# Optimization experiments

Measured on AMD Instinct MI355X. Metric: run time of the kernel, lower is better.

Reference implementation:

```python
import jax, jax.numpy as jnp
import numpy as np

N = 50000
E = 800000
IN_FEAT = 128
HEADS = 2
HEAD_DIM = 64  # hidden_feat // num_heads for 'concat'
HIDDEN = HEADS * HEAD_DIM
N_CLASSES = 16
NEG_SLOPE = 0.2
BN_EPS = 1e-5


def setup_inputs() -> dict:
    key = jax.random.key(0)
    ks = jax.random.split(key, 20)
    s = 0.1  # weight scale for numerical sanity
    return {
        "x": jax.random.normal(ks[0], (N, IN_FEAT), jnp.float32),
        "src0": jax.random.randint(ks[1], (E,), 0, N, jnp.int32),
        "dst0": jax.random.randint(ks[2], (E,), 0, N, jnp.int32),
        "ew0": jax.random.uniform(ks[3], (E,), jnp.float32),
        "src1": jax.random.randint(ks[4], (E,), 0, N, jnp.int32),
        "dst1": jax.random.randint(ks[5], (E,), 0, N, jnp.int32),
        "ew1": jax.random.uniform(ks[6], (E,), jnp.float32),
        "fc_w0": jax.random.normal(ks[7], (HIDDEN, IN_FEAT), jnp.float32) * s,
        "bias0": jnp.zeros((HIDDEN,), jnp.float32),
        "attn_l0": jax.random.normal(ks[8], (HEADS, HEAD_DIM), jnp.float32) * s,
        "attn_r0": jax.random.normal(ks[9], (HEADS, HEAD_DIM), jnp.float32) * s,
        "fc_w1": jax.random.normal(ks[10], (HIDDEN, IN_FEAT), jnp.float32) * s,
        "bias1": jnp.zeros((HIDDEN,), jnp.float32),
        "attn_l1": jax.random.normal(ks[11], (HEADS, HEAD_DIM), jnp.float32) * s,
        "attn_r1": jax.random.normal(ks[12], (HEADS, HEAD_DIM), jnp.float32) * s,
        "skip_w": jax.random.normal(ks[13], (HIDDEN, IN_FEAT), jnp.float32) * s,
        "skip_b": jnp.zeros((HIDDEN,), jnp.float32),
        "bn_gamma": jnp.ones((HIDDEN,), jnp.float32),
        "bn_beta": jnp.zeros((HIDDEN,), jnp.float32),
        "clf_w": jax.random.normal(ks[14], (N_CLASSES, HIDDEN), jnp.float32) * s,
        "clf_b": jnp.zeros((N_CLASSES,), jnp.float32),
    }


def _weighted_gat(x, src, dst, ew, fc_w, bias, attn_l, attn_r):
    # DGL GATConv with per-edge weight scaling of attention.
    f = (x @ fc_w.T).reshape(N, HEADS, HEAD_DIM)          # [N,H,D]
    el = jnp.sum(f * attn_l, axis=-1)                      # [N,H]
    er = jnp.sum(f * attn_r, axis=-1)                      # [N,H]
    e = jax.nn.leaky_relu(el[src] + er[dst], NEG_SLOPE)    # [E,H]
    # edge softmax over incoming edges of each dst, numerically stable
    m = jax.ops.segment_max(e, dst, num_segments=N)        # [N,H]
    ex = jnp.exp(e - m[dst])
    den = jax.ops.segment_sum(ex, dst, num_segments=N)     # [N,H]
    alpha = ex / den[dst]                                  # [E,H]
    alpha = alpha * ew[:, None]                            # edge-weight scaling
    msg = alpha[..., None] * f[src]                        # [E,H,D]
    out = jax.ops.segment_sum(msg, dst, num_segments=N)    # [N,H,D]
    return out + bias.reshape(1, HEADS, HEAD_DIM)


def reference(x, src0, dst0, ew0, src1, dst1, ew1,
              fc_w0, bias0, attn_l0, attn_r0,
              fc_w1, bias1, attn_l1, attn_r1,
              skip_w, skip_b, bn_gamma, bn_beta, clf_w, clf_b):
    # HeteroGraphConv with aggregate='sum': sum per-relation GAT outputs
    h2 = _weighted_gat(x, src0, dst0, ew0, fc_w0, bias0, attn_l0, attn_r0) \
       + _weighted_gat(x, src1, dst1, ew1, fc_w1, bias1, attn_l1, attn_r1)
    # multihead 'concat' aggregate with relu: flatten heads
    h2 = jax.nn.relu(h2).reshape(N, HIDDEN)
    # linear skip + residual add (dropout is identity at eval)
    h = (x @ skip_w.T + skip_b) + h2
    # classifier: BatchNorm1d (batch stats) -> ReLU -> Linear
    mu = jnp.mean(h, axis=0)
    var = jnp.mean((h - mu) ** 2, axis=0)
    hn = (h - mu) * jax.lax.rsqrt(var + BN_EPS) * bn_gamma + bn_beta
    logits = jax.nn.relu(hn) @ clf_w.T + clf_b
    return logits
```

## Files before the change

### kernel.cpp

```cpp
#include <hip/hip_runtime.h>
#include <hip/hip_bf16.h>

#define N_NODES 50000
#define N_EDGES 800000
#define HID 128
#define NEG_SLOPE 0.2f
#define BN_EPS 1e-5f

#define NBLK 256
#define BINSZ 512
#define BINSH 9
#define NBINS 98

typedef __bf16 v8bf __attribute__((ext_vector_type(8)));
typedef float v4f __attribute__((ext_vector_type(4)));

__device__ __forceinline__ float leaky(float v) {
    return (v > 0.f) ? v : v * NEG_SLOPE;
}
__device__ __forceinline__ unsigned int f2bu(float f) {
    __hip_bfloat16 b = __float2bfloat16(f);
    return (unsigned int)*reinterpret_cast<unsigned short*>(&b);
}
__device__ __forceinline__ unsigned int pack2bf(float lo, float hi) {
    return f2bu(lo) | (f2bu(hi) << 16);
}

__global__ __launch_bounds__(256) void k_prepw(const float* __restrict__ w0,
                                               const float* __restrict__ w1,
                                               const float* __restrict__ wsk,
                                               unsigned short* __restrict__ wb) {
    const int WQ = 128 * 128 / 4;
    int q = blockIdx.x * 256 + threadIdx.x;
    if (q >= 3 * WQ) return;
    int mat = q >> 12;
    int rem = q & 4095;
    const float* W = (mat == 0) ? w0 : (mat == 1) ? w1 : wsk;
    float4 v = ((const float4*)W)[rem];
    ushort4 o;
    o.x = (unsigned short)f2bu(v.x);
    o.y = (unsigned short)f2bu(v.y);
    o.z = (unsigned short)f2bu(v.z);
    o.w = (unsigned short)f2bu(v.w);
    *(ushort4*)(wb + (size_t)mat * 16384 + rem * 4) = o;
}

__global__ __launch_bounds__(256) void k_bincount(const int* __restrict__ dst0,
                                                  const int* __restrict__ dst1,
                                                  int* __restrict__ bincnt) {
    int rel = blockIdx.y;
    const int* dst = rel ? dst1 : dst0;
    __shared__ int cnt[NBINS];
    for (int i = threadIdx.x; i < NBINS; i += 256) cnt[i] = 0;
    __syncthreads();
    const int CH = (N_EDGES + NBLK - 1) / NBLK;
    int b0 = blockIdx.x * CH;
    int b1 = min(N_EDGES, b0 + CH);
    for (int e = b0 + threadIdx.x; e < b1; e += 256)
        atomicAdd(&cnt[dst[e] >> BINSH], 1);
    __syncthreads();
    for (int i = threadIdx.x; i < NBINS; i += 256)
        bincnt[rel * NBINS * NBLK + i * NBLK + blockIdx.x] = cnt[i];
}

__global__ __launch_bounds__(1024) void k_binscan(int* __restrict__ bincnt) {
    int* a = bincnt + blockIdx.x * NBINS * NBLK;
    const int TOT = NBINS * NBLK;
    const int CH = (TOT + 1023) / 1024;
    int tid = threadIdx.x;
    int base = tid * CH;
    int lv[CH];
    int sum = 0;
    for (int i = 0; i < CH; i++) {
        int idx = base + i;
        int v = (idx < TOT) ? a[idx] : 0;
        lv[i] = sum;
        sum += v;
    }
    __shared__ int ls[1024];
    ls[tid] = sum;
    __syncthreads();
    for (int ofs = 1; ofs < 1024; ofs <<= 1) {
        int v = (tid >= ofs) ? ls[tid - ofs] : 0;
        __syncthreads();
        ls[tid] += v;
        __syncthreads();
    }
    int pre = tid ? ls[tid - 1] : 0;
    for (int i = 0; i < CH; i++) {
        int idx = base + i;
        if (idx < TOT) a[idx] = pre + lv[i];
    }
}

__global__ __launch_bounds__(256) void k_binscatter(const int* __restrict__ dst0,
                                                    const int* __restrict__ dst1,
                                                    const int* __restrict__ src0,
                                                    const int* __restrict__ src1,
                                                    const float* __restrict__ ew0,
                                                    const float* __restrict__ ew1,
                                                    const int* __restrict__ bincnt,
                                                    int2* __restrict__ pairs0,
                                                    int2* __restrict__ pairs1) {
    int rel = blockIdx.y;
    const int* dst = rel ? dst1 : dst0;
    const int* src = rel ? src1 : src0;
    const float* ew = rel ? ew1 : ew0;
    int2* pairs = rel ? pairs1 : pairs0;
    __shared__ int cur[NBINS];
    for (int i = threadIdx.x; i < NBINS; i += 256)
        cur[i] = bincnt[rel * NBINS * NBLK + i * NBLK + blockIdx.x];
    __syncthreads();
    const int CH = (N_EDGES + NBLK - 1) / NBLK;
    int b0 = blockIdx.x * CH;
    int b1 = min(N_EDGES, b0 + CH);
    for (int e = b0 + threadIdx.x; e < b1; e += 256) {
        int d = dst[e];
        int pos = atomicAdd(&cur[d >> BINSH], 1);
        unsigned int packed = (unsigned int)(d & (BINSZ - 1)) |
                              ((unsigned int)src[e] << BINSH);
        pairs[pos] = make_int2((int)packed, __float_as_int(ew[e]));
    }
}

__global__ __launch_bounds__(256) void k_csr(const int* __restrict__ bincnt,
                                             const int2* __restrict__ pairs0,
                                             const int2* __restrict__ pairs1,
                                             const float* __restrict__ el0,
                                             const float* __restrict__ el1,
                                             int* __restrict__ offs0,
                                             int* __restrict__ offs1,
                                             int4* __restrict__ rec0,
                                             int4* __restrict__ rec1) {
    int rel = blockIdx.y;
    const int2* pairs = rel ? pairs1 : pairs0;
    const float* el = rel ? el1 : el0;
    int* offs = rel ? offs1 : offs0;
    int4* rec = rel ? rec1 : rec0;
    int bin = blockIdx.x;
    int tid = threadIdx.x;
    const int* bc = bincnt + rel * NBINS * NBLK;
    int pbase = bc[bin * NBLK];
    int pend = (bin < NBINS - 1) ? bc[(bin + 1) * NBLK] : N_EDGES;
    int n0 = bin << BINSH;
    int nn = min(N_NODES - n0, BINSZ);

    __shared__ int s_deg[BINSZ];
    __shared__ int s_ts[256];
    for (int i = tid; i < BINSZ; i += 256) s_deg[i] = 0;
    __syncthreads();
    for (int p = pbase + tid; p < pend; p += 256)
        atomicAdd(&s_deg[((unsigned int)pairs[p].x) & (BINSZ - 1)], 1);
    __syncthreads();

    int d0 = s_deg[tid * 2], d1 = s_deg[tid * 2 + 1];
    s_ts[tid] = d0 + d1;
    __syncthreads();
    for (int ofs = 1; ofs < 256; ofs <<= 1) {
        int v = (tid >= ofs) ? s_ts[tid - ofs] : 0;
        __syncthreads();
        s_ts[tid] += v;
        __syncthreads();
    }
    int pre = tid ? s_ts[tid - 1] : 0;
    s_deg[tid * 2] = pbase + pre;
    s_deg[tid * 2 + 1] = pbase + pre + d0;
    __syncthreads();

    for (int l = tid; l < nn; l += 256) offs[n0 + l] = s_deg[l];
    if (bin == NBINS - 1 && tid == 0) offs[N_NODES] = N_EDGES;
    __syncthreads();

    for (int p = pbase + tid; p < pend; p += 256) {
        int2 pr = pairs[p];
        unsigned int u = (unsigned int)pr.x;
        int dl = (int)(u & (BINSZ - 1));
        int s = (int)(u >> BINSH);
        int pos = atomicAdd(&s_deg[dl], 1);
        float2 ev = *(const float2*)(el + 2 * s);
        rec[pos] = make_int4(s << 8, pr.y,
                             __float_as_int(ev.x), __float_as_int(ev.y));
    }
}

__global__ __launch_bounds__(256) void k_gemm_mfma(
    const float* __restrict__ x, const unsigned short* __restrict__ wb,
    const float* __restrict__ skip_b,
    const float* __restrict__ al0, const float* __restrict__ ar0,
    const float* __restrict__ al1, const float* __restrict__ ar1,
    unsigned short* __restrict__ fb0, unsigned short* __restrict__ fb1,
    float* __restrict__ el0, float* __restrict__ er0,
    float* __restrict__ el1, float* __restrict__ er1,
    float* __restrict__ hs) {
    __shared__ unsigned short As[64][128];
    __shared__ unsigned short Bs[64][128];
    int tid = threadIdx.x;
    int m0 = blockIdx.x * 64;

#pragma unroll
    for (int i = 0; i < 4; i++) {
        int idx = tid * 4 + i;
        int row = idx >> 4, seg = idx & 15;
        int gr = m0 + row;
        uint4 o = make_uint4(0, 0, 0, 0);
        if (gr < N_NODES) {
            const float* p = x + (size_t)gr * HID + seg * 8;
            float4 p0 = *(const float4*)p;
            float4 p1 = *(const float4*)(p + 4);
            o.x = pack2bf(p0.x, p0.y);
            o.y = pack2bf(p0.z, p0.w);
            o.z = pack2bf(p1.x, p1.y);
            o.w = pack2bf(p1.z, p1.w);
        }
        *(uint4*)(&As[row][(seg ^ (row & 7)) * 8]) = o;
    }
    __syncthreads();

    int w = tid >> 6, l = tid & 63;
    int lr = l & 15, lg = l >> 4;
    int node = m0 + w * 16 + lr;
    bool valid = node < N_NODES;
    int arow = w * 16 + lr;
    v8bf afrag[4];
#pragma unroll
    for (int kb = 0; kb < 4; kb++)
        afrag[kb] = *(v8bf*)(&As[arow][((kb * 4 + lg) ^ (arow & 7)) * 8]);

    for (int s = 0; s < 6; s++) {
        int mat = s >> 1;
        int j0 = (s & 1) * 64;
        const unsigned short* wmat = wb + (size_t)mat * 16384 + j0 * HID;
        __syncthreads();
#pragma unroll
        for (int i = 0; i < 4; i++) {
            int idx = tid * 4 + i;
            int row = idx >> 4, seg = idx & 15;
            uint4 wv = *(const uint4*)(wmat + row * HID + seg * 8);
            *(uint4*)(&Bs[row][(seg ^ (row & 7)) * 8]) = wv;
        }
        __syncthreads();

        v4f acc[4] = {};
#pragma unroll
        for (int nt = 0; nt < 4; nt++) {
            int brow = nt * 16 + lr;
#pragma unroll
            for (int kb = 0; kb < 4; kb++) {
                v8bf bfrag =
                    *(v8bf*)(&Bs[brow][((kb * 4 + lg) ^ (brow & 7)) * 8]);
                acc[nt] = __builtin_amdgcn_mfma_f32_16x16x32_bf16(
                    bfrag, afrag[kb], acc[nt], 0, 0, 0);
            }
        }

        if (mat < 2) {
            int h = s & 1;
            const float* al = mat ? al1 : al0;
            const float* ar = mat ? ar1 : ar0;
            float* elp = mat ? el1 : el0;
            float* erp = mat ? er1 : er0;
            unsigned short* fbp = mat ? fb1 : fb0;
            float elv = 0.f, erv = 0.f;
#pragma unroll
            for (int nt = 0; nt < 4; nt++) {
                int c0 = j0 + nt * 16 + lg * 4;
                float4 av = *(const float4*)(al + c0);
                float4 rv = *(const float4*)(ar + c0);
                elv += acc[nt][0] * av.x + acc[nt][1] * av.y +
                       acc[nt][2] * av.z + acc[nt][3] * av.w;
                erv += acc[nt][0] * rv.x + acc[nt][1] * rv.y +
                       acc[nt][2] * rv.z + acc[nt][3] * rv.w;
            }
            elv += __shfl_xor(elv, 16);
            elv += __shfl_xor(elv, 32);
            erv += __shfl_xor(erv, 16);
            erv += __shfl_xor(erv, 32);
            if (valid) {
#pragma unroll
                for (int nt = 0; nt < 4; nt++) {
                    uint2 o;
                    o.x = pack2bf(acc[nt][0], acc[nt][1]);
                    o.y = pack2bf(acc[nt][2], acc[nt][3]);
                    *(uint2*)(fbp + (size_t)node * HID + j0 + nt * 16 + lg * 4) = o;
                }
                if (lg == 0) {
                    elp[node * 2 + h] = elv;
                    erp[node * 2 + h] = erv;
                }
            }
        } else if (valid) {
#pragma unroll
            for (int nt = 0; nt < 4; nt++) {
                int c0 = j0 + nt * 16 + lg * 4;
                float4 sb = *(const float4*)(skip_b + c0);
                float4 o;
                o.x = acc[nt][0] + sb.x;
                o.y = acc[nt][1] + sb.y;
                o.z = acc[nt][2] + sb.z;
                o.w = acc[nt][3] + sb.w;
                *(float4*)(hs + (size_t)node * HID + c0) = o;
            }
        }
    }
}

__device__ __forceinline__ void agg_rel2(const int* __restrict__ offs,
                                         const int4* __restrict__ rec,
                                         const float* __restrict__ er,
                                         const unsigned char* __restrict__ fbb,
                                         int n, int lane, int sub8,
                                         int hh, float* a) {
    int b = offs[n];
    int e_end = offs[n + 1];
    int deg = e_end - b;
    if (deg <= 0) return;
    float ern0 = er[2 * n], ern1 = er[2 * n + 1];

    const int NC = 4;
    int cs[NC];
    float cw0[NC], cw1[NC];
    unsigned int cpk[NC];
    float d0 = 0.f, d1 = 0.f;
    int nchunk = (deg + 63) >> 6;
    for (int ch = 0; ch < nchunk; ch++) {
        int p = b + (ch << 6) + lane;
        int s = 0;
        float w0 = 0.f, w1 = 0.f;
        if (p < e_end) {
            int4 r = rec[p];
            s = r.x;
            float wgt = __int_as_float(r.y);
            float x0 = expf(leaky(__int_as_float(r.z) + ern0));
            float x1 = expf(leaky(__int_as_float(r.w) + ern1));
            d0 += x0;
            d1 += x1;
            w0 = x0 * wgt;
            w1 = x1 * wgt;
        }
        if (ch < NC) {
            cs[ch] = s;
            cw0[ch] = w0;
            cw1[ch] = w1;
        }
    }
#pragma unroll
    for (int m = 32; m; m >>= 1) {
        d0 += __shfl_xor(d0, m);
        d1 += __shfl_xor(d1, m);
    }
    float inv0 = 1.f / d0, inv1 = 1.f / d1;
#pragma unroll
    for (int ch = 0; ch < NC; ch++)
        cpk[ch] = pack2bf(cw0[ch] * inv0, cw1[ch] * inv1);

    for (int ch = 0; ch < nchunk; ch++) {
        int s;
        unsigned int pk;
        if (ch < NC) {
            s = cs[ch];
            pk = cpk[ch];
        } else {
            int p = b + (ch << 6) + lane;
            s = 0;
            pk = 0;
            if (p < e_end) {
                int4 r = rec[p];
                s = r.x;
                float wgt = __int_as_float(r.y);
                float w0 = expf(leaky(__int_as_float(r.z) + ern0)) * wgt;
                float w1 = expf(leaky(__int_as_float(r.w) + ern1)) * wgt;
                pk = pack2bf(w0 * inv0, w1 * inv1);
            }
        }
        int cnt = deg - (ch << 6);
        if (cnt > 64) cnt = 64;
        int ng = (cnt + 7) >> 3;
#pragma unroll 2
        for (int g = 0; g < ng; g++) {
            int sl = (g << 3) + sub8;
            int sj = __shfl(s, sl);
            unsigned int pkj = (unsigned int)__shfl((int)pk, sl);
            float aj = __uint_as_float(hh ? (pkj & 0xffff0000u) : (pkj << 16));
            uint4 f0 = *(const uint4*)(fbb + sj);
            uint4 f1 = *(const uint4*)(fbb + sj + 16);
            a[0]  += aj * __uint_as_float(f0.x << 16);
            a[1]  += aj * __uint_as_float(f0.x & 0xffff0000u);
            a[2]  += aj * __uint_as_float(f0.y << 16);
            a[3]  += aj * __uint_as_float(f0.y & 0xffff0000u);
            a[4]  += aj * __uint_as_float(f0.z << 16);
            a[5]  += aj * __uint_as_float(f0.z & 0xffff0000u);
            a[6]  += aj * __uint_as_float(f0.w << 16);
            a[7]  += aj * __uint_as_float(f0.w & 0xffff0000u);
            a[8]  += aj * __uint_as_float(f1.x << 16);
            a[9]  += aj * __uint_as_float(f1.x & 0xffff0000u);
            a[10] += aj * __uint_as_float(f1.y << 16);
            a[11] += aj * __uint_as_float(f1.y & 0xffff0000u);
            a[12] += aj * __uint_as_float(f1.z << 16);
            a[13] += aj * __uint_as_float(f1.z & 0xffff0000u);
            a[14] += aj * __uint_as_float(f1.w << 16);
            a[15] += aj * __uint_as_float(f1.w & 0xffff0000u);
        }
    }
}

__global__ __launch_bounds__(256) void k_aggregate(
    const int* __restrict__ offs0, const int4* __restrict__ rec0,
    const float* __restrict__ er0, const unsigned short* __restrict__ fb0,
    const int* __restrict__ offs1, const int4* __restrict__ rec1,
    const float* __restrict__ er1, const unsigned short* __restrict__ fb1,
    const float* __restrict__ bias0, const float* __restrict__ bias1,
    float* __restrict__ h) {
    int wave = threadIdx.x >> 6, lane = threadIdx.x & 63;
    int n = blockIdx.x * 4 + wave;
    if (n >= N_NODES) return;
    int cb8 = lane & 7;
    int sub8 = lane >> 3;
    int hh = cb8 >> 2;
    float a[16] = {};
    const unsigned char* fbb0 = (const unsigned char*)fb0 + cb8 * 32;
    const unsigned char* fbb1 = (const unsigned char*)fb1 + cb8 * 32;
    agg_rel2(offs0, rec0, er0, fbb0, n, lane, sub8, hh, a);
    agg_rel2(offs1, rec1, er1, fbb1, n, lane, sub8, hh, a);
#pragma unroll
    for (int j = 0; j < 16; j++) {
        a[j] += __shfl_xor(a[j], 8);
        a[j] += __shfl_xor(a[j], 16);
        a[j] += __shfl_xor(a[j], 32);
    }
    if (sub8 == 0) {
        int c0 = cb8 * 16;
        size_t base = (size_t)n * HID + c0;
#pragma unroll
        for (int q = 0; q < 4; q++) {
            float4 v = *(const float4*)(h + base + q * 4);
            float4 b0 = *(const float4*)(bias0 + c0 + q * 4);
            float4 b1 = *(const float4*)(bias1 + c0 + q * 4);
            float4 o;
            o.x = v.x + fmaxf(a[q * 4 + 0] + b0.x + b1.x, 0.f);
            o.y = v.y + fmaxf(a[q * 4 + 1] + b0.y + b1.y, 0.f);
            o.z = v.z + fmaxf(a[q * 4 + 2] + b0.z + b1.z, 0.f);
            o.w = v.w + fmaxf(a[q * 4 + 3] + b0.w + b1.w, 0.f);
            *(float4*)(h + base + q * 4) = o;
        }
    }
}

__global__ __launch_bounds__(256) void k_bnstats(const float* __restrict__ h,
                                                 double* __restrict__ psum,
                                                 double* __restrict__ psumsq) {
    int tid = threadIdx.x;
    const float4* h4 = (const float4*)h;
    double s[4] = {0.0, 0.0, 0.0, 0.0};
    double q[4] = {0.0, 0.0, 0.0, 0.0};
    const int totalv = N_NODES * HID / 4;
    const int stride = 512 * 256;
    for (int i = blockIdx.x * 256 + tid; i < totalv; i += stride) {
        float4 v = h4[i];
        s[0] += v.x; q[0] += (double)v.x * v.x;
        s[1] += v.y; q[1] += (double)v.y * v.y;
        s[2] += v.z; q[2] += (double)v.z * v.z;
        s[3] += v.w; q[3] += (double)v.w * v.w;
    }
    __shared__ double ls[256][4], lq[256][4];
#pragma unroll
    for (int j = 0; j < 4; j++) {
        ls[tid][j] = s[j];
        lq[tid][j] = q[j];
    }
    __syncthreads();
    if (tid < 32) {
#pragma unroll
        for (int j = 0; j < 4; j++) {
            double ss = 0.0, qq = 0.0;
            for (int t = tid; t < 256; t += 32) {
                ss += ls[t][j];
                qq += lq[t][j];
            }
            psum[blockIdx.x * 128 + tid * 4 + j] = ss;
            psumsq[blockIdx.x * 128 + tid * 4 + j] = qq;
        }
    }
}

__global__ void k_bn_finalize(const double* __restrict__ psum,
                              const double* __restrict__ psumsq,
                              const float* __restrict__ gamma,
                              const float* __restrict__ beta,
                              float* __restrict__ ss) {
    int c = threadIdx.x;
    double s = 0.0, q = 0.0;
    for (int b = 0; b < 512; b++) {
        s += psum[b * 128 + c];
        q += psumsq[b * 128 + c];
    }
    double mu = s / N_NODES;
    double var = q / N_NODES - mu * mu;
    float sc = gamma[c] * (float)(1.0 / sqrt(var + (double)BN_EPS));
    ss[c] = sc;
    ss[128 + c] = beta[c] - (float)mu * sc;
}

__global__ __launch_bounds__(256) void k_classify(const float* __restrict__ h,
                                                  const float* __restrict__ ss,
                                                  const float* __restrict__ clf_w,
                                                  const float* __restrict__ clf_b,
                                                  float* __restrict__ out) {
    int w = threadIdx.x >> 6, l = threadIdx.x & 63;
    int lr = l & 15, lg = l >> 4;
    int n0 = (blockIdx.x * 4 + w) * 16;
    if (n0 >= N_NODES) return;

    v8bf afrag[4], bfrag[4];
#pragma unroll
    for (int kb = 0; kb < 4; kb++) {
        int k0 = kb * 32 + lg * 8;
        const float* bp = clf_w + lr * HID + k0;
        float4 b0 = *(const float4*)bp;
        float4 b1 = *(const float4*)(bp + 4);
        bfrag[kb][0] = (__bf16)b0.x; bfrag[kb][1] = (__bf16)b0.y;
        bfrag[kb][2] = (__bf16)b0.z; bfrag[kb][3] = (__bf16)b0.w;
        bfrag[kb][4] = (__bf16)b1.x; bfrag[kb][5] = (__bf16)b1.y;
        bfrag[kb][6] = (__bf16)b1.z; bfrag[kb][7] = (__bf16)b1.w;
        const float* ap = h + (size_t)(n0 + lr) * HID + k0;
        float4 a0 = *(const float4*)ap;
        float4 a1 = *(const float4*)(ap + 4);
        float4 sc0 = *(const float4*)(ss + k0);
        float4 sc1 = *(const float4*)(ss + k0 + 4);
        float4 sh0 = *(const float4*)(ss + 128 + k0);
        float4 sh1 = *(const float4*)(ss + 128 + k0 + 4);
        afrag[kb][0] = (__bf16)fmaxf(a0.x * sc0.x + sh0.x, 0.f);
        afrag[kb][1] = (__bf16)fmaxf(a0.y * sc0.y + sh0.y, 0.f);
        afrag[kb][2] = (__bf16)fmaxf(a0.z * sc0.z + sh0.z, 0.f);
        afrag[kb][3] = (__bf16)fmaxf(a0.w * sc0.w + sh0.w, 0.f);
        afrag[kb][4] = (__bf16)fmaxf(a1.x * sc1.x + sh1.x, 0.f);
        afrag[kb][5] = (__bf16)fmaxf(a1.y * sc1.y + sh1.y, 0.f);
        afrag[kb][6] = (__bf16)fmaxf(a1.z * sc1.z + sh1.z, 0.f);
        afrag[kb][7] = (__bf16)fmaxf(a1.w * sc1.w + sh1.w, 0.f);
    }
    v4f acc = {};
#pragma unroll
    for (int kb = 0; kb < 4; kb++)
        acc = __builtin_amdgcn_mfma_f32_16x16x32_bf16(bfrag[kb], afrag[kb],
                                                      acc, 0, 0, 0);
    float4 cb = *(const float4*)(clf_b + lg * 4);
    float4 o;
    o.x = acc[0] + cb.x;
    o.y = acc[1] + cb.y;
    o.z = acc[2] + cb.z;
    o.w = acc[3] + cb.w;
    *(float4*)(out + (size_t)(n0 + lr) * 16 + lg * 4) = o;
}

extern "C" void kernel_launch(void* const* d_in, const int* in_sizes, int n_in,
                              void* d_out, int out_size, void* d_ws, size_t ws_size,
                              hipStream_t stream) {
    (void)in_sizes; (void)n_in; (void)out_size; (void)ws_size;
    const float* x      = (const float*)d_in[0];
    const int*   src0   = (const int*)d_in[1];
    const int*   dst0   = (const int*)d_in[2];
    const float* ew0    = (const float*)d_in[3];
    const int*   src1   = (const int*)d_in[4];
    const int*   dst1   = (const int*)d_in[5];
    const float* ew1    = (const float*)d_in[6];
    const float* fc_w0  = (const float*)d_in[7];
    const float* bias0  = (const float*)d_in[8];
    const float* al0    = (const float*)d_in[9];
    const float* ar0    = (const float*)d_in[10];
    const float* fc_w1  = (const float*)d_in[11];
    const float* bias1  = (const float*)d_in[12];
    const float* al1    = (const float*)d_in[13];
    const float* ar1    = (const float*)d_in[14];
    const float* skip_w = (const float*)d_in[15];
    const float* skip_b = (const float*)d_in[16];
    const float* gamma  = (const float*)d_in[17];
    const float* beta   = (const float*)d_in[18];
    const float* clf_w  = (const float*)d_in[19];
    const float* clf_b  = (const float*)d_in[20];
    float* out = (float*)d_out;

    char* wsp = (char*)d_ws;
    size_t off = 0;
    auto alloc = [&](size_t bytes) -> char* {
        char* p = wsp + off;
        off += (bytes + 255) & ~(size_t)255;
        return p;
    };
    unsigned short* wbf = (unsigned short*)alloc((size_t)3 * 16384 * 2);
    unsigned short* fb0 = (unsigned short*)alloc((size_t)N_NODES * HID * 2);
    unsigned short* fb1 = (unsigned short*)alloc((size_t)N_NODES * HID * 2);
    float*  hs     = (float*)alloc((size_t)N_NODES * HID * 4);
    float*  el0    = (float*)alloc((size_t)N_NODES * 2 * 4);
    float*  er0    = (float*)alloc((size_t)N_NODES * 2 * 4);
    float*  el1    = (float*)alloc((size_t)N_NODES * 2 * 4);
    float*  er1    = (float*)alloc((size_t)N_NODES * 2 * 4);
    int*    bincnt = (int*)alloc((size_t)2 * NBINS * NBLK * 4);
    int2*   pairs0 = (int2*)alloc((size_t)N_EDGES * 8);
    int2*   pairs1 = (int2*)alloc((size_t)N_EDGES * 8);
    int*    offs0  = (int*)alloc((size_t)(N_NODES + 1) * 4);
    int*    offs1  = (int*)alloc((size_t)(N_NODES + 1) * 4);
    int4*   rec0   = (int4*)alloc((size_t)N_EDGES * 16);
    int4*   rec1   = (int4*)alloc((size_t)N_EDGES * 16);
    double* psum   = (double*)alloc((size_t)512 * 128 * 8);
    double* psumsq = (double*)alloc((size_t)512 * 128 * 8);
    float*  ss     = (float*)alloc(256 * 4);

    k_prepw<<<48, 256, 0, stream>>>(fc_w0, fc_w1, skip_w, wbf);

    dim3 gbin(NBLK, 2);
    k_bincount<<<gbin, 256, 0, stream>>>(dst0, dst1, bincnt);
    k_binscan<<<2, 1024, 0, stream>>>(bincnt);
    k_binscatter<<<gbin, 256, 0, stream>>>(dst0, dst1, src0, src1, ew0, ew1,
                                           bincnt, pairs0, pairs1);

    k_gemm_mfma<<<(N_NODES + 63) / 64, 256, 0, stream>>>(
        x, wbf, skip_b, al0, ar0, al1, ar1,
        fb0, fb1, el0, er0, el1, er1, hs);

    dim3 gcsr(NBINS, 2);
    k_csr<<<gcsr, 256, 0, stream>>>(bincnt, pairs0, pairs1, el0, el1,
                                    offs0, offs1, rec0, rec1);

    k_aggregate<<<(N_NODES + 3) / 4, 256, 0, stream>>>(
        offs0, rec0, er0, fb0, offs1, rec1, er1, fb1, bias0, bias1, hs);

    k_bnstats<<<512, 256, 0, stream>>>(hs, psum, psumsq);
    k_bn_finalize<<<1, 128, 0, stream>>>(psum, psumsq, gamma, beta, ss);
    k_classify<<<(N_NODES + 63) / 64, 256, 0, stream>>>(
        hs, ss, clf_w, clf_b, out);
}
```

Before: 231.2 us.

## Precompute softmax numerators and denominators in CSR build, shrink edge records

Moves the edge exp(leaky(el+er)) computation and the per-destination softmax denominator accumulation into the CSR construction kernel, using shared-memory atomics. The edge record shrinks from 16 to 8 bytes by storing bf16-packed weighted numerators. The aggregation kernel becomes a single pass per chunk, with no second rec read or reduction. It also rebalances lanes to 16 columns by 4 edge groups with 16-byte gathers. The cost is that numerators are rounded to bf16 before normalization, and k_csr does extra shared atomics and er loads.

```diff
diff --git a/kernel.cpp b/kernel.cpp
--- a/kernel.cpp
+++ b/kernel.cpp
@@ -127,16 +127,22 @@
                                              const int2* __restrict__ pairs0,
                                              const int2* __restrict__ pairs1,
                                              const float* __restrict__ el0,
+                                             const float* __restrict__ er0,
                                              const float* __restrict__ el1,
+                                             const float* __restrict__ er1,
                                              int* __restrict__ offs0,
                                              int* __restrict__ offs1,
-                                             int4* __restrict__ rec0,
-                                             int4* __restrict__ rec1) {
+                                             int2* __restrict__ rec0,
+                                             int2* __restrict__ rec1,
+                                             float2* __restrict__ den20,
+                                             float2* __restrict__ den21) {
     int rel = blockIdx.y;
     const int2* pairs = rel ? pairs1 : pairs0;
     const float* el = rel ? el1 : el0;
+    const float* er = rel ? er1 : er0;
     int* offs = rel ? offs1 : offs0;
-    int4* rec = rel ? rec1 : rec0;
+    int2* rec = rel ? rec1 : rec0;
+    float2* den2 = rel ? den21 : den20;
     int bin = blockIdx.x;
     int tid = threadIdx.x;
     const int* bc = bincnt + rel * NBINS * NBLK;
@@ -147,7 +153,9 @@
 
     __shared__ int s_deg[BINSZ];
     __shared__ int s_ts[256];
+    __shared__ float sden[BINSZ * 2];
     for (int i = tid; i < BINSZ; i += 256) s_deg[i] = 0;
+    for (int i = tid; i < BINSZ * 2; i += 256) sden[i] = 0.f;
     __syncthreads();
     for (int p = pbase + tid; p < pend; p += 256)
         atomicAdd(&s_deg[((unsigned int)pairs[p].x) & (BINSZ - 1)], 1);
@@ -178,9 +186,17 @@
         int s = (int)(u >> BINSH);
         int pos = atomicAdd(&s_deg[dl], 1);
         float2 ev = *(const float2*)(el + 2 * s);
-        rec[pos] = make_int4(s << 8, pr.y,
-                             __float_as_int(ev.x), __float_as_int(ev.y));
-    }
+        float2 rv = *(const float2*)(er + 2 * (n0 + dl));
+        float x0 = expf(leaky(ev.x + rv.x));
+        float x1 = expf(leaky(ev.y + rv.y));
+        atomicAdd(&sden[dl * 2], x0);
+        atomicAdd(&sden[dl * 2 + 1], x1);
+        float ew = __int_as_float(pr.y);
+        rec[pos] = make_int2(s << 8, (int)pack2bf(x0 * ew, x1 * ew));
+    }
+    __syncthreads();
+    for (int l = tid; l < nn; l += 256)
+        den2[n0 + l] = make_float2(sden[l * 2], sden[l * 2 + 1]);
 }
 
 __global__ __launch_bounds__(256) void k_gemm_mfma(
@@ -305,143 +321,91 @@
 }
 
 __device__ __forceinline__ void agg_rel2(const int* __restrict__ offs,
-                                         const int4* __restrict__ rec,
-                                         const float* __restrict__ er,
+                                         const int2* __restrict__ rec,
+                                         const float2* __restrict__ den2,
                                          const unsigned char* __restrict__ fbb,
-                                         int n, int lane, int sub8,
+                                         int n, int lane, int sub,
                                          int hh, float* a) {
     int b = offs[n];
     int e_end = offs[n + 1];
     int deg = e_end - b;
     if (deg <= 0) return;
-    float ern0 = er[2 * n], ern1 = er[2 * n + 1];
-
-    const int NC = 4;
-    int cs[NC];
-    float cw0[NC], cw1[NC];
-    unsigned int cpk[NC];
-    float d0 = 0.f, d1 = 0.f;
+    float2 dn = den2[n];
+    float inv0 = 1.f / dn.x, inv1 = 1.f / dn.y;
+
     int nchunk = (deg + 63) >> 6;
     for (int ch = 0; ch < nchunk; ch++) {
         int p = b + (ch << 6) + lane;
         int s = 0;
-        float w0 = 0.f, w1 = 0.f;
+        unsigned int wpk = 0;
         if (p < e_end) {
-            int4 r = rec[p];
+            int2 r = rec[p];
             s = r.x;
-            float wgt = __int_as_float(r.y);
-            float x0 = expf(leaky(__int_as_float(r.z) + ern0));
-            float x1 = expf(leaky(__int_as_float(r.w) + ern1));
-            d0 += x0;
-            d1 += x1;
-            w0 = x0 * wgt;
-            w1 = x1 * wgt;
-        }
-        if (ch < NC) {
-            cs[ch] = s;
-            cw0[ch] = w0;
-            cw1[ch] = w1;
-        }
-    }
-#pragma unroll
-    for (int m = 32; m; m >>= 1) {
-        d0 += __shfl_xor(d0, m);
-        d1 += __shfl_xor(d1, m);
-    }
-    float inv0 = 1.f / d0, inv1 = 1.f / d1;
-#pragma unroll
-    for (int ch = 0; ch < NC; ch++)
-        cpk[ch] = pack2bf(cw0[ch] * inv0, cw1[ch] * inv1);
-
-    for (int ch = 0; ch < nchunk; ch++) {
-        int s;
-        unsigned int pk;
-        if (ch < NC) {
-            s = cs[ch];
-            pk = cpk[ch];
-        } else {
-            int p = b + (ch << 6) + lane;
-            s = 0;
-            pk = 0;
-            if (p < e_end) {
-                int4 r = rec[p];
-                s = r.x;
-                float wgt = __int_as_float(r.y);
-                float w0 = expf(leaky(__int_as_float(r.z) + ern0)) * wgt;
-                float w1 = expf(leaky(__int_as_float(r.w) + ern1)) * wgt;
-                pk = pack2bf(w0 * inv0, w1 * inv1);
-            }
-        }
+            wpk = (unsigned int)r.y;
+        }
+        unsigned int pk = pack2bf(__uint_as_float(wpk << 16) * inv0,
+                                  __uint_as_float(wpk & 0xffff0000u) * inv1);
         int cnt = deg - (ch << 6);
         if (cnt > 64) cnt = 64;
-        int ng = (cnt + 7) >> 3;
+        int ng = (cnt + 3) >> 2;
 #pragma unroll 2
         for (int g = 0; g < ng; g++) {
-            int sl = (g << 3) + sub8;
+            int sl = (g << 2) + sub;
             int sj = __shfl(s, sl);
             unsigned int pkj = (unsigned int)__shfl((int)pk, sl);
             float aj = __uint_as_float(hh ? (pkj & 0xffff0000u) : (pkj << 16));
-            uint4 f0 = *(const uint4*)(fbb + sj);
-            uint4 f1 = *(const uint4*)(fbb + sj + 16);
-            a[0]  += aj * __uint_as_float(f0.x << 16);
-            a[1]  += aj * __uint_as_float(f0.x & 0xffff0000u);
-            a[2]  += aj * __uint_as_float(f0.y << 16);
-            a[3]  += aj * __uint_as_float(f0.y & 0xffff0000u);
-            a[4]  += aj * __uint_as_float(f0.z << 16);
-            a[5]  += aj * __uint_as_float(f0.z & 0xffff0000u);
-            a[6]  += aj * __uint_as_float(f0.w << 16);
-            a[7]  += aj * __uint_as_float(f0.w & 0xffff0000u);
-            a[8]  += aj * __uint_as_float(f1.x << 16);
-            a[9]  += aj * __uint_as_float(f1.x & 0xffff0000u);
-            a[10] += aj * __uint_as_float(f1.y << 16);
-            a[11] += aj * __uint_as_float(f1.y & 0xffff0000u);
-            a[12] += aj * __uint_as_float(f1.z << 16);
-            a[13] += aj * __uint_as_float(f1.z & 0xffff0000u);
-            a[14] += aj * __uint_as_float(f1.w << 16);
-            a[15] += aj * __uint_as_float(f1.w & 0xffff0000u);
+            uint4 fv = *(const uint4*)(fbb + sj);
+            a[0] += aj * __uint_as_float(fv.x << 16);
+            a[1] += aj * __uint_as_float(fv.x & 0xffff0000u);
+            a[2] += aj * __uint_as_float(fv.y << 16);
+            a[3] += aj * __uint_as_float(fv.y & 0xffff0000u);
+            a[4] += aj * __uint_as_float(fv.z << 16);
+            a[5] += aj * __uint_as_float(fv.z & 0xffff0000u);
+            a[6] += aj * __uint_as_float(fv.w << 16);
+            a[7] += aj * __uint_as_float(fv.w & 0xffff0000u);
         }
     }
 }
 
 __global__ __launch_bounds__(256) void k_aggregate(
-    const int* __restrict__ offs0, const int4* __restrict__ rec0,
-    const float* __restrict__ er0, const unsigned short* __restrict__ fb0,
-    const int* __restrict__ offs1, const int4* __restrict__ rec1,
-    const float* __restrict__ er1, const unsigned short* __restrict__ fb1,
+    const int* __restrict__ offs0, const int2* __restrict__ rec0,
+    const float2* __restrict__ den20, const unsigned short* __restrict__ fb0,
+    const int* __restrict__ offs1, const int2* __restrict__ rec1,
+    const float2* __restrict__ den21, const unsigned short* __restrict__ fb1,
     const float* __restrict__ bias0, const float* __restrict__ bias1,
     float* __restrict__ h) {
     int wave = threadIdx.x >> 6, lane = threadIdx.x & 63;
     int n = blockIdx.x * 4 + wave;
     if (n >= N_NODES) return;
-    int cb8 = lane & 7;
-    int sub8 = lane >> 3;
-    int hh = cb8 >> 2;
-    float a[16] = {};
-    const unsigned char* fbb0 = (const unsigned char*)fb0 + cb8 * 32;
-    const unsigned char* fbb1 = (const unsigned char*)fb1 + cb8 * 32;
-    agg_rel2(offs0, rec0, er0, fbb0, n, lane, sub8, hh, a);
-    agg_rel2(offs1, rec1, er1, fbb1, n, lane, sub8, hh, a);
-#pragma unroll
-    for (int j = 0; j < 16; j++) {
-        a[j] += __shfl_xor(a[j], 8);
+    int cb = lane & 15;
+    int sub = lane >> 4;
+    int hh = cb >> 3;
+    float a[8] = {0.f, 0.f, 0.f, 0.f, 0.f, 0.f, 0.f, 0.f};
+    const unsigned char* fbb0 = (const unsigned char*)fb0 + cb * 16;
+    const unsigned char* fbb1 = (const unsigned char*)fb1 + cb * 16;
+    agg_rel2(offs0, rec0, den20, fbb0, n, lane, sub, hh, a);
+    agg_rel2(offs1, rec1, den21, fbb1, n, lane, sub, hh, a);
+#pragma unroll
+    for (int j = 0; j < 8; j++) {
         a[j] += __shfl_xor(a[j], 16);
         a[j] += __shfl_xor(a[j], 32);
     }
-    if (sub8 == 0) {
-        int c0 = cb8 * 16;
-        size_t base = (size_t)n * HID + c0;
-#pragma unroll
-        for (int q = 0; q < 4; q++) {
-            float4 v = *(const float4*)(h + base + q * 4);
-            float4 b0 = *(const float4*)(bias0 + c0 + q * 4);
-            float4 b1 = *(const float4*)(bias1 + c0 + q * 4);
-            float4 o;
-            o.x = v.x + fmaxf(a[q * 4 + 0] + b0.x + b1.x, 0.f);
-            o.y = v.y + fmaxf(a[q * 4 + 1] + b0.y + b1.y, 0.f);
-            o.z = v.z + fmaxf(a[q * 4 + 2] + b0.z + b1.z, 0.f);
-            o.w = v.w + fmaxf(a[q * 4 + 3] + b0.w + b1.w, 0.f);
-            *(float4*)(h + base + q * 4) = o;
-        }
+    if (sub == 0) {
+        size_t base = (size_t)n * HID + cb * 8;
+        float4 v0 = *(const float4*)(h + base);
+        float4 v1 = *(const float4*)(h + base + 4);
+        int c0 = cb * 8;
+        float4 o0, o1;
+        o0.x = v0.x + fmaxf(a[0] + bias0[c0 + 0] + bias1[c0 + 0], 0.f);
+        o0.y = v0.y + fmaxf(a[1] + bias0[c0 + 1] + bias1[c0 + 1], 0.f);
+        o0.z = v0.z + fmaxf(a[2] + bias0[c0 + 2] + bias1[c0 + 2], 0.f);
+        o0.w = v0.w + fmaxf(a[3] + bias0[c0 + 3] + bias1[c0 + 3], 0.f);
+        o1.x = v1.x + fmaxf(a[4] + bias0[c0 + 4] + bias1[c0 + 4], 0.f);
+        o1.y = v1.y + fmaxf(a[5] + bias0[c0 + 5] + bias1[c0 + 5], 0.f);
+        o1.z = v1.z + fmaxf(a[6] + bias0[c0 + 6] + bias1[c0 + 6], 0.f);
+        o1.w = v1.w + fmaxf(a[7] + bias0[c0 + 7] + bias1[c0 + 7], 0.f);
+        *(float4*)(h + base) = o0;
+        *(float4*)(h + base + 4) = o1;
     }
 }
 
@@ -598,8 +562,10 @@
     int2*   pairs1 = (int2*)alloc((size_t)N_EDGES * 8);
     int*    offs0  = (int*)alloc((size_t)(N_NODES + 1) * 4);
     int*    offs1  = (int*)alloc((size_t)(N_NODES + 1) * 4);
-    int4*   rec0   = (int4*)alloc((size_t)N_EDGES * 16);
-    int4*   rec1   = (int4*)alloc((size_t)N_EDGES * 16);
+    int2*   rec0   = (int2*)alloc((size_t)N_EDGES * 8);
+    int2*   rec1   = (int2*)alloc((size_t)N_EDGES * 8);
+    float2* den20  = (float2*)alloc((size_t)N_NODES * 8);
+    float2* den21  = (float2*)alloc((size_t)N_NODES * 8);
     double* psum   = (double*)alloc((size_t)512 * 128 * 8);
     double* psumsq = (double*)alloc((size_t)512 * 128 * 8);
     float*  ss     = (float*)alloc(256 * 4);
@@ -617,11 +583,12 @@
         fb0, fb1, el0, er0, el1, er1, hs);
 
     dim3 gcsr(NBINS, 2);
-    k_csr<<<gcsr, 256, 0, stream>>>(bincnt, pairs0, pairs1, el0, el1,
-                                    offs0, offs1, rec0, rec1);
+    k_csr<<<gcsr, 256, 0, stream>>>(bincnt, pairs0, pairs1,
+                                    el0, er0, el1, er1,
+                                    offs0, offs1, rec0, rec1, den20, den21);
 
     k_aggregate<<<(N_NODES + 3) / 4, 256, 0, stream>>>(
-        offs0, rec0, er0, fb0, offs1, rec1, er1, fb1, bias0, bias1, hs);
+        offs0, rec0, den20, fb0, offs1, rec1, den21, fb1, bias0, bias1, hs);
 
     k_bnstats<<<512, 256, 0, stream>>>(hs, psum, psumsq);
     k_bn_finalize<<<1, 128, 0, stream>>>(psum, psumsq, gamma, beta, ss);
```

Measured after the change: 228.5 us. No clear change (-1.2%).
